# Optimization experiments

Hardware: AMD Instinct MI355X
Metric: run time of the kernel (lower is better)

Reference implementation:

```python
import jax, jax.numpy as jnp
import numpy as np

LOSS1_COEFF = 1.0
LOSS2_COEFF = 1.0
LOSS3_COEFF = 1.0
LOSS4_COEFF = 0.5


def smooth_l1(x, y):
    # torch smooth_l1_loss, beta=1, reduction='mean'
    d = jnp.abs(x - y)
    return jnp.mean(jnp.where(d < 1.0, 0.5 * d * d, d - 0.5))


def setup_inputs() -> dict:
    key = jax.random.key(0)
    k1, k2 = jax.random.split(key)
    B, N, F = 256, 8192, 13
    targets = jax.random.uniform(k1, (B, N, F), dtype=jnp.float32)
    preds = jax.random.uniform(k2, (B, N, F), dtype=jnp.float32)
    return {"targets": targets, "preds": preds}


def reference(targets, preds):
    tb = targets[:, :, :4]  # [B,N,4]
    pb = preds[:, :, :4]
    # The original builds a [B,N,N] pairwise IoU matrix and takes its diagonal;
    # the diagonal is exactly the elementwise matched-pair IoU, computed here directly.
    xx1 = jnp.maximum(tb[..., 0], pb[..., 0])
    yy1 = jnp.maximum(tb[..., 1], pb[..., 1])
    xx2 = jnp.minimum(tb[..., 2], pb[..., 2])
    yy2 = jnp.minimum(tb[..., 3], pb[..., 3])
    w = jnp.clip(xx2 - xx1, 0.0)
    h = jnp.clip(yy2 - yy1, 0.0)
    inter = w * h
    area1 = (tb[..., 2] - tb[..., 0]) * (tb[..., 3] - tb[..., 1])
    area2 = (pb[..., 2] - pb[..., 0]) * (pb[..., 3] - pb[..., 1])
    ious = inter / (area1 + area2 - inter + 1e-07)  # [B,N]

    loss1 = smooth_l1(jnp.ones_like(ious), ious)
    loss2 = smooth_l1(tb, pb)
    loss3 = smooth_l1(targets[:, :, -1], preds[:, :, -1])
    loss4 = smooth_l1(targets[:, :, 4:12], preds[:, :, 4:12])
    return (LOSS1_COEFF * loss1 + LOSS2_COEFF * loss2
            + LOSS3_COEFF * loss3 + LOSS4_COEFF * loss4)
```

## Files before the change

kernel.cpp:

```cpp
#include <hip/hip_runtime.h>
#include <hip/hip_bf16.h>


#define NCHUNK 8192
#define RPC    256
#define FPC    (RPC * 13)
#define SEGS   13
#define NBLK   768

typedef const __attribute__((address_space(1))) float gfloat;
typedef __attribute__((address_space(3))) float lfloat;

__device__ __forceinline__ float sl1(float d) {
    d = fabsf(d);
    return d < 1.0f ? 0.5f * d * d : d - 0.5f;
}

__global__ __launch_bounds__(256) void loss_stage1(const float* __restrict__ T,
                                                   const float* __restrict__ P,
                                                   float* __restrict__ partial) {
    __shared__ float st[2][FPC];
    __shared__ float sp[2][FPC];
    __shared__ float wred[4];

    const int tid  = threadIdx.x;
    const int lane = tid & 63;
    const int wv   = tid >> 6;

    auto stage = [&](int c, int b) {
        const long long gb = (long long)c * FPC + lane * 4;
        for (int s = wv; s < SEGS; s += 4) {
            __builtin_amdgcn_global_load_lds((gfloat*)(T + gb + s * 256),
                                             (lfloat*)&st[b][s * 256 + lane * 4],
                                             16, 0, 0);
            __builtin_amdgcn_global_load_lds((gfloat*)(P + gb + s * 256),
                                             (lfloat*)&sp[b][s * 256 + lane * 4],
                                             16, 0, 0);
        }
    };

    int c   = blockIdx.x;
    int cur = 0;
    float acc = 0.0f;

    stage(c, 0);

    for (; c < NCHUNK; c += NBLK) {
        __syncthreads();

        const int cn = c + NBLK;
        if (cn < NCHUNK) stage(cn, cur ^ 1);

        const float* t = st[cur];
        const float* p = sp[cur];
        const int rb = tid * 13;

        float t0 = t[rb+0], t1 = t[rb+1], t2 = t[rb+2], t3 = t[rb+3];
        float p0 = p[rb+0], p1 = p[rb+1], p2 = p[rb+2], p3 = p[rb+3];

        float s2 = sl1(t0-p0) + sl1(t1-p1) + sl1(t2-p2) + sl1(t3-p3);

        float s4 = 0.0f;
#pragma unroll
        for (int f = 4; f < 12; ++f) s4 += sl1(t[rb+f] - p[rb+f]);

        float s3 = sl1(t[rb+12] - p[rb+12]);

        float xx1 = fmaxf(t0, p0);
        float yy1 = fmaxf(t1, p1);
        float xx2 = fminf(t2, p2);
        float yy2 = fminf(t3, p3);
        float w  = fmaxf(xx2 - xx1, 0.0f);
        float h  = fmaxf(yy2 - yy1, 0.0f);
        float inter = w * h;
        float a1 = (t2 - t0) * (t3 - t1);
        float a2 = (p2 - p0) * (p3 - p1);
        float iou = inter / (a1 + a2 - inter + 1e-7f);
        float s1 = sl1(1.0f - iou);

        constexpr float W1 = 1.0f / 2097152.0f;
        constexpr float W2 = 1.0f / 8388608.0f;
        constexpr float W3 = 1.0f / 2097152.0f;
        constexpr float W4 = 1.0f / 33554432.0f;
        acc += W1*s1 + W2*s2 + W3*s3 + W4*s4;

        cur ^= 1;
    }

#pragma unroll
    for (int off = 32; off > 0; off >>= 1)
        acc += __shfl_down(acc, off, 64);
    if (lane == 0) wred[wv] = acc;
    __syncthreads();
    if (tid == 0)
        partial[blockIdx.x] = wred[0] + wred[1] + wred[2] + wred[3];
}

__global__ __launch_bounds__(256) void loss_stage2(const float* __restrict__ partial,
                                                   float* __restrict__ out) {
    __shared__ float wred[4];
    const int tid = threadIdx.x;
    float a = 0.0f;
    for (int i = tid; i < NBLK; i += 256) a += partial[i];
#pragma unroll
    for (int off = 32; off > 0; off >>= 1)
        a += __shfl_down(a, off, 64);
    if ((tid & 63) == 0) wred[tid >> 6] = a;
    __syncthreads();
    if (tid == 0) out[0] = wred[0] + wred[1] + wred[2] + wred[3];
}

extern "C" void kernel_launch(void* const* d_in, const int* in_sizes, int n_in,
                              void* d_out, int out_size, void* d_ws, size_t ws_size,
                              hipStream_t stream) {
    const float* targets = (const float*)d_in[0];
    const float* preds   = (const float*)d_in[1];
    float* out     = (float*)d_out;
    float* partial = (float*)d_ws;

    loss_stage1<<<NBLK, 256, 0, stream>>>(targets, preds, partial);
    loss_stage2<<<1, 256, 0, stream>>>(partial, out);
}
```

Baseline: 228.7 us.

## Stage data per wave with explicit vmcnt waits instead of block barriers

Each wavefront now owns a private double-buffered LDS region and stages its own 64-row group through global_load_lds. Progress is tracked with s_waitcnt vmcnt counts rather than __syncthreads, so the per-iteration block barrier goes away. Two loads are put in flight up front, and the grid changes from 768 blocks to 512. The risk is the hand-counted vmcnt value and issuing the refill into the same buffer right after it is read, which relies on LDS reads having completed first.

```diff
diff --git a/kernel.cpp b/kernel.cpp
--- a/kernel.cpp
+++ b/kernel.cpp
@@ -1,12 +1,13 @@
 #include <hip/hip_runtime.h>
-#include <hip/hip_bf16.h>
 
 
-#define NCHUNK 8192
-#define RPC    256
-#define FPC    (RPC * 13)
-#define SEGS   13
-#define NBLK   768
+#define NGRP   32768
+#define GBYTES 3328
+#define GFLOAT 832
+#define NBUF   2
+#define NBLK   512
+#define NWAVE  (NBLK * 4)
+#define GPW    (NGRP / NWAVE)
 
 typedef const __attribute__((address_space(1))) float gfloat;
 typedef __attribute__((address_space(3))) float lfloat;
@@ -19,52 +20,57 @@
 __global__ __launch_bounds__(256) void loss_stage1(const float* __restrict__ T,
                                                    const float* __restrict__ P,
                                                    float* __restrict__ partial) {
-    __shared__ float st[2][FPC];
-    __shared__ float sp[2][FPC];
+    __shared__ float lds[4][NBUF][2][GFLOAT];
     __shared__ float wred[4];
 
     const int tid  = threadIdx.x;
     const int lane = tid & 63;
     const int wv   = tid >> 6;
+    const int wid  = blockIdx.x * 4 + wv;
 
-    auto stage = [&](int c, int b) {
-        const long long gb = (long long)c * FPC + lane * 4;
-        for (int s = wv; s < SEGS; s += 4) {
-            __builtin_amdgcn_global_load_lds((gfloat*)(T + gb + s * 256),
-                                             (lfloat*)&st[b][s * 256 + lane * 4],
-                                             16, 0, 0);
-            __builtin_amdgcn_global_load_lds((gfloat*)(P + gb + s * 256),
-                                             (lfloat*)&sp[b][s * 256 + lane * 4],
-                                             16, 0, 0);
+    auto stage = [&](int g, int b) {
+        const char* tb = (const char*)T + (long long)g * GBYTES;
+        const char* pb = (const char*)P + (long long)g * GBYTES;
+        lfloat* lt = (lfloat*)&lds[wv][b][0][0];
+        lfloat* lp = (lfloat*)&lds[wv][b][1][0];
+#pragma unroll
+        for (int s = 0; s < 3; ++s) {
+            __builtin_amdgcn_global_load_lds((gfloat*)(tb + s * 1024 + lane * 16),
+                                             lt + s * 256 + lane * 4, 16, 0, 0);
+            __builtin_amdgcn_global_load_lds((gfloat*)(pb + s * 1024 + lane * 16),
+                                             lp + s * 256 + lane * 4, 16, 0, 0);
         }
+        __builtin_amdgcn_global_load_lds((gfloat*)(tb + 3072 + lane * 4),
+                                         lt + 768 + lane, 4, 0, 0);
+        __builtin_amdgcn_global_load_lds((gfloat*)(pb + 3072 + lane * 4),
+                                         lp + 768 + lane, 4, 0, 0);
     };
 
-    int c   = blockIdx.x;
-    int cur = 0;
+    stage(wid, 0);
+    stage(wid + NWAVE, 1);
+
     float acc = 0.0f;
 
-    stage(c, 0);
+    for (int i = 0; i < GPW; ++i) {
+        if (i < GPW - 1) asm volatile("s_waitcnt vmcnt(8)" ::: "memory");
+        else             asm volatile("s_waitcnt vmcnt(0)" ::: "memory");
+        __builtin_amdgcn_sched_barrier(0);
 
-    for (; c < NCHUNK; c += NBLK) {
-        __syncthreads();
+        const int buf = i & 1;
+        const float* t = &lds[wv][buf][0][0];
+        const float* p = &lds[wv][buf][1][0];
+        const int rb = lane * 13;
 
-        const int cn = c + NBLK;
-        if (cn < NCHUNK) stage(cn, cur ^ 1);
+        float t0 = t[rb + 0], t1 = t[rb + 1], t2 = t[rb + 2], t3 = t[rb + 3];
+        float p0 = p[rb + 0], p1 = p[rb + 1], p2 = p[rb + 2], p3 = p[rb + 3];
 
-        const float* t = st[cur];
-        const float* p = sp[cur];
-        const int rb = tid * 13;
-
-        float t0 = t[rb+0], t1 = t[rb+1], t2 = t[rb+2], t3 = t[rb+3];
-        float p0 = p[rb+0], p1 = p[rb+1], p2 = p[rb+2], p3 = p[rb+3];
-
-        float s2 = sl1(t0-p0) + sl1(t1-p1) + sl1(t2-p2) + sl1(t3-p3);
+        float s2 = sl1(t0 - p0) + sl1(t1 - p1) + sl1(t2 - p2) + sl1(t3 - p3);
 
         float s4 = 0.0f;
 #pragma unroll
-        for (int f = 4; f < 12; ++f) s4 += sl1(t[rb+f] - p[rb+f]);
+        for (int f = 4; f < 12; ++f) s4 += sl1(t[rb + f] - p[rb + f]);
 
-        float s3 = sl1(t[rb+12] - p[rb+12]);
+        float s3 = sl1(t[rb + 12] - p[rb + 12]);
 
         float xx1 = fmaxf(t0, p0);
         float yy1 = fmaxf(t1, p1);
@@ -82,9 +88,9 @@
         constexpr float W2 = 1.0f / 8388608.0f;
         constexpr float W3 = 1.0f / 2097152.0f;
         constexpr float W4 = 1.0f / 33554432.0f;
-        acc += W1*s1 + W2*s2 + W3*s3 + W4*s4;
+        acc += W1 * s1 + W2 * s2 + W3 * s3 + W4 * s4;
 
-        cur ^= 1;
+        if (i + 2 < GPW) stage(wid + (i + 2) * NWAVE, buf);
     }
 
 #pragma unroll
```

New measurement: 227.5 us. About the same (-0.5%).

## Replace LDS double-buffered staging with direct float4 register loads per 4-row quad

Applied to the files above, without the earlier changes.

Removes the async global-to-LDS double-buffer pipeline. Each thread now loads 4 consecutive rows (52 floats) straight into registers as 13 float4 loads per input, avoiding LDS traffic, per-chunk barriers and bank conflicts on the stride-13 LDS reads. The grid goes from 768 to 1024 blocks with a fixed two iterations per thread. Each thread's float4 loads hit scattered 208-byte blocks rather than coalesced rows, and the wider per-thread state raises register pressure, which may reduce occupancy.

```diff
diff --git a/kernel.cpp b/kernel.cpp
--- a/kernel.cpp
+++ b/kernel.cpp
@@ -1,80 +1,49 @@
 #include <hip/hip_runtime.h>
-#include <hip/hip_bf16.h>
 
 
-#define NCHUNK 8192
-#define RPC    256
-#define FPC    (RPC * 13)
-#define SEGS   13
-#define NBLK   768
+#define NQUAD  524288
+#define NBLK   1024
+#define NTHR   (NBLK * 256)
+#define QPT    (NQUAD / NTHR)
 
-typedef const __attribute__((address_space(1))) float gfloat;
-typedef __attribute__((address_space(3))) float lfloat;
+#define GETC(v, c) ((c) == 0 ? (v).x : (c) == 1 ? (v).y : (c) == 2 ? (v).z : (v).w)
+#define GET(arr, idx) GETC(arr[(idx) >> 2], (idx) & 3)
 
 __device__ __forceinline__ float sl1(float d) {
     d = fabsf(d);
     return d < 1.0f ? 0.5f * d * d : d - 0.5f;
 }
 
-__global__ __launch_bounds__(256) void loss_stage1(const float* __restrict__ T,
-                                                   const float* __restrict__ P,
-                                                   float* __restrict__ partial) {
-    __shared__ float st[2][FPC];
-    __shared__ float sp[2][FPC];
-    __shared__ float wred[4];
+__device__ __forceinline__ float quad_loss(const float4* a, const float4* b) {
+    float acc = 0.0f;
+#pragma unroll
+    for (int r = 0; r < 4; ++r) {
+        float t[13], p[13];
+#pragma unroll
+        for (int f = 0; f < 13; ++f) {
+            const int idx = r * 13 + f;
+            t[f] = GET(a, idx);
+            p[f] = GET(b, idx);
+        }
 
-    const int tid  = threadIdx.x;
-    const int lane = tid & 63;
-    const int wv   = tid >> 6;
-
-    auto stage = [&](int c, int b) {
-        const long long gb = (long long)c * FPC + lane * 4;
-        for (int s = wv; s < SEGS; s += 4) {
-            __builtin_amdgcn_global_load_lds((gfloat*)(T + gb + s * 256),
-                                             (lfloat*)&st[b][s * 256 + lane * 4],
-                                             16, 0, 0);
-            __builtin_amdgcn_global_load_lds((gfloat*)(P + gb + s * 256),
-                                             (lfloat*)&sp[b][s * 256 + lane * 4],
-                                             16, 0, 0);
-        }
-    };
-
-    int c   = blockIdx.x;
-    int cur = 0;
-    float acc = 0.0f;
-
-    stage(c, 0);
-
-    for (; c < NCHUNK; c += NBLK) {
-        __syncthreads();
-
-        const int cn = c + NBLK;
-        if (cn < NCHUNK) stage(cn, cur ^ 1);
-
-        const float* t = st[cur];
-        const float* p = sp[cur];
-        const int rb = tid * 13;
-
-        float t0 = t[rb+0], t1 = t[rb+1], t2 = t[rb+2], t3 = t[rb+3];
-        float p0 = p[rb+0], p1 = p[rb+1], p2 = p[rb+2], p3 = p[rb+3];
-
-        float s2 = sl1(t0-p0) + sl1(t1-p1) + sl1(t2-p2) + sl1(t3-p3);
+        float s2 = sl1(t[0] - p[0]) + sl1(t[1] - p[1]) +
+                   sl1(t[2] - p[2]) + sl1(t[3] - p[3]);
 
         float s4 = 0.0f;
 #pragma unroll
-        for (int f = 4; f < 12; ++f) s4 += sl1(t[rb+f] - p[rb+f]);
+        for (int f = 4; f < 12; ++f) s4 += sl1(t[f] - p[f]);
 
-        float s3 = sl1(t[rb+12] - p[rb+12]);
+        float s3 = sl1(t[12] - p[12]);
 
-        float xx1 = fmaxf(t0, p0);
-        float yy1 = fmaxf(t1, p1);
-        float xx2 = fminf(t2, p2);
-        float yy2 = fminf(t3, p3);
+        float xx1 = fmaxf(t[0], p[0]);
+        float yy1 = fmaxf(t[1], p[1]);
+        float xx2 = fminf(t[2], p[2]);
+        float yy2 = fminf(t[3], p[3]);
         float w  = fmaxf(xx2 - xx1, 0.0f);
         float h  = fmaxf(yy2 - yy1, 0.0f);
         float inter = w * h;
-        float a1 = (t2 - t0) * (t3 - t1);
-        float a2 = (p2 - p0) * (p3 - p1);
+        float a1 = (t[2] - t[0]) * (t[3] - t[1]);
+        float a2 = (p[2] - p[0]) * (p[3] - p[1]);
         float iou = inter / (a1 + a2 - inter + 1e-7f);
         float s1 = sl1(1.0f - iou);
 
@@ -82,15 +51,36 @@
         constexpr float W2 = 1.0f / 8388608.0f;
         constexpr float W3 = 1.0f / 2097152.0f;
         constexpr float W4 = 1.0f / 33554432.0f;
-        acc += W1*s1 + W2*s2 + W3*s3 + W4*s4;
+        acc += W1 * s1 + W2 * s2 + W3 * s3 + W4 * s4;
+    }
+    return acc;
+}
 
-        cur ^= 1;
+__global__ __launch_bounds__(256) void loss_stage1(const float* __restrict__ T,
+                                                   const float* __restrict__ P,
+                                                   float* __restrict__ partial) {
+    __shared__ float wred[4];
+    const int tid  = threadIdx.x;
+    const int gtid = blockIdx.x * 256 + tid;
+
+    float acc = 0.0f;
+#pragma unroll
+    for (int it = 0; it < QPT; ++it) {
+        const long long q = gtid + (long long)it * NTHR;
+        const float4* tq = (const float4*)(T + q * 52);
+        const float4* pq = (const float4*)(P + q * 52);
+
+        float4 a[13], b[13];
+#pragma unroll
+        for (int k = 0; k < 13; ++k) { a[k] = tq[k]; b[k] = pq[k]; }
+
+        acc += quad_loss(a, b);
     }
 
 #pragma unroll
     for (int off = 32; off > 0; off >>= 1)
         acc += __shfl_down(acc, off, 64);
-    if (lane == 0) wred[wv] = acc;
+    if ((tid & 63) == 0) wred[tid >> 6] = acc;
     __syncthreads();
     if (tid == 0)
         partial[blockIdx.x] = wred[0] + wred[1] + wred[2] + wred[3];
```

Measured after the change: 263.0 us. +15.0%, slower.
